# Optimization experiments

Hardware: AMD Instinct MI355X
Metric: run time of the kernel (lower is better)

The kernel has to match this reference:

```python
import jax, jax.numpy as jnp
import numpy as np

N, F = 8000, 256
NEG_SLOPE = 0.2


def setup_inputs() -> dict:
    key = jax.random.key(0)
    k1, k2, k3, k4, k5, k6, k7 = jax.random.split(key, 7)
    node_embeddings = jax.random.normal(k1, (N, F), dtype=jnp.float32)
    adj_matrix = jax.random.randint(k2, (N, N), 0, 2, dtype=jnp.int32)
    # Learned params: W (Linear F->F with bias), a (Linear 2F->1 with bias).
    # a's weight [1, 2F] is split into a_src (first F, applied to H_i) and
    # a_dst (last F, applied to H_j) -- mathematically identical to the
    # concat-then-linear formulation, without the N*N*2F intermediate.
    s = 1.0 / np.sqrt(F)
    W_w = jax.random.uniform(k3, (F, F), dtype=jnp.float32, minval=-s, maxval=s)
    W_b = jax.random.uniform(k4, (F,), dtype=jnp.float32, minval=-s, maxval=s)
    s2 = 1.0 / np.sqrt(2 * F)
    a_src = jax.random.uniform(k5, (F,), dtype=jnp.float32, minval=-s2, maxval=s2)
    a_dst = jax.random.uniform(k6, (F,), dtype=jnp.float32, minval=-s2, maxval=s2)
    a_b = jax.random.uniform(k7, (), dtype=jnp.float32, minval=-s2, maxval=s2)
    return {
        "node_embeddings": node_embeddings,
        "adj_matrix": adj_matrix,
        "W_w": W_w,
        "W_b": W_b,
        "a_src": a_src,
        "a_dst": a_dst,
        "a_b": a_b,
    }


def reference(node_embeddings, adj_matrix, W_w, W_b, a_src, a_dst, a_b):
    # H = W(x)
    H = node_embeddings @ W_w.T + W_b                      # [N, F]
    # e_ij = a([H_i ; H_j]) = H_i . a_src + H_j . a_dst + b
    e = (H @ a_src)[:, None] + (H @ a_dst)[None, :] + a_b  # [N, N]
    # mask BEFORE leakyrelu (as in the original), then leakyrelu, then softmax
    e = jnp.where(adj_matrix == 0, -jnp.inf, e)
    e = jnp.where(e >= 0, e, NEG_SLOPE * e)                # leakyrelu(-inf) = -inf
    attn = jax.nn.softmax(e, axis=1)                       # [N, N]
    return attn @ H                                        # [N, F]
```

## Files before the change

kernel.cpp:

```cpp
#include <hip/hip_runtime.h>

#define NN 8000
#define FD 256
#define NEG_SLOPE 0.2f
#define BM 64
#define KT 32
#define JCH 2048

typedef __bf16 bf16;
typedef __bf16 bf16x8 __attribute__((ext_vector_type(8)));
typedef __bf16 bf16x4 __attribute__((ext_vector_type(4)));
typedef float f32x4 __attribute__((ext_vector_type(4)));

__global__ __launch_bounds__(256) void k_linear(const float* __restrict__ X,
                                                const float* __restrict__ W,
                                                const float* __restrict__ b,
                                                bf16* __restrict__ Ht,
                                                float* __restrict__ out,
                                                float* __restrict__ lg) {
    __shared__ float Xs[16][260];
    const int t = threadIdx.x;
    const int i0 = blockIdx.x * 16;
    {
        const int gt = blockIdx.x * 256 + t;
        const float4 z4 = {0.f, 0.f, 0.f, 0.f};
        float4* o4 = (float4*)out;
        #pragma unroll
        for (int k = 0; k < 4; ++k) o4[gt + k * 128000] = z4;
        if (gt < NN) lg[gt] = 0.f;
    }
    #pragma unroll
    for (int r = 0; r < 16; ++r)
        Xs[r][t] = X[(size_t)(i0 + r) * FD + t];
    __syncthreads();
    const int f = t;
    float acc[16];
    const float bf_ = b[f];
    #pragma unroll
    for (int ii = 0; ii < 16; ++ii) acc[ii] = bf_;
    for (int k4 = 0; k4 < FD / 4; ++k4) {
        const float4 w4 = *(const float4*)&W[(size_t)f * FD + k4 * 4];
        #pragma unroll
        for (int ii = 0; ii < 16; ++ii) {
            const float4 x4 = *(const float4*)&Xs[ii][k4 * 4];
            acc[ii] += x4.x * w4.x + x4.y * w4.y + x4.z * w4.z + x4.w * w4.w;
        }
    }
    bf16x8 v0, v1;
    #pragma unroll
    for (int ii = 0; ii < 8; ++ii) { v0[ii] = (bf16)acc[ii]; v1[ii] = (bf16)acc[ii + 8]; }
    *(bf16x8*)&Ht[(size_t)f * NN + i0]     = v0;
    *(bf16x8*)&Ht[(size_t)f * NN + i0 + 8] = v1;
}

__global__ __launch_bounds__(256) void k_attn_vec(const bf16* __restrict__ Ht,
                                                  const float* __restrict__ a_src,
                                                  const float* __restrict__ a_dst,
                                                  const float* __restrict__ a_b,
                                                  float* __restrict__ hs,
                                                  float* __restrict__ hd) {
    __shared__ float psh[4][64], pdh[4][64];
    const int t = threadIdx.x;
    const int li = t & 63;
    const int q = t >> 6;
    const int i = blockIdx.x * 64 + li;
    float ps = 0.f, pd = 0.f;
    #pragma unroll 8
    for (int fi = 0; fi < 64; ++fi) {
        const int f = q * 64 + fi;
        const float h = (float)Ht[(size_t)f * NN + i];
        ps += h * a_src[f];
        pd += h * a_dst[f];
    }
    psh[q][li] = ps; pdh[q][li] = pd;
    __syncthreads();
    if (q == 0) {
        ps = psh[0][li] + psh[1][li] + psh[2][li] + psh[3][li];
        pd = pdh[0][li] + pdh[1][li] + pdh[2][li] + pdh[3][li];
        hs[i] = ps + a_b[0];
        hd[i] = pd;
    }
}

__global__ __launch_bounds__(512, 2) void k_gat(const bf16* __restrict__ Ht,
                                                const int* __restrict__ adj,
                                                const float* __restrict__ hs,
                                                const float* __restrict__ hd,
                                                float* __restrict__ out,
                                                float* __restrict__ lg) {
    __shared__ __attribute__((aligned(16))) bf16 Bt[2][FD * KT];
    __shared__ __attribute__((aligned(16))) int  Adt[3][BM * KT];
    __shared__ __attribute__((aligned(16))) bf16 Wt[2][BM * 40];
    __shared__ float hd_s[JCH];

    const int t  = threadIdx.x;
    const int l  = t & 63;
    const int wv = t >> 6;
    const int jb = blockIdx.x & 3;
    const int ib = blockIdx.x >> 2;
    const int i0 = ib * BM;
    const int j0 = jb * JCH;
    const int NS = (jb < 3) ? 64 : 58;

    const int r  = t >> 3;
    const int js = t & 7;
    const float hsv = hs[i0 + r];

    const int is = wv >> 2, fg = wv & 3;
    const int al = l & 15, asl = l >> 4;
    const int bswz = (asl ^ ((al >> 2) & 3)) << 4;

    auto stage_bt = [&](int s_, int buf) {
        #pragma unroll
        for (int q = 0; q < 2; ++q) {
            const int idx = q * 512 + t;
            const int col = idx >> 2, ks = idx & 3;
            const bf16* src = Ht + (size_t)col * NN + j0 + s_ * KT
                              + ((ks ^ ((col >> 2) & 3)) * 8);
            bf16* dst = &Bt[buf][idx * 8];
            __builtin_amdgcn_global_load_lds(
                (const __attribute__((address_space(1))) void*)src,
                (__attribute__((address_space(3))) void*)dst, 16, 0, 0);
        }
    };
    auto stage_ad = [&](int s_, int buf) {
        const int* src = adj + (size_t)(i0 + r) * NN + j0 + s_ * KT + js * 4;
        int* dst = &Adt[buf][t * 4];
        __builtin_amdgcn_global_load_lds(
            (const __attribute__((address_space(1))) void*)src,
            (__attribute__((address_space(3))) void*)dst, 16, 0, 0);
    };

    {
        const int jg = j0 + t * 4;
        float4 h4 = {0.f, 0.f, 0.f, 0.f};
        if (jg + 3 < NN) h4 = *(const float4*)(hd + jg);
        *(float4*)&hd_s[t * 4] = h4;
    }
    asm volatile("s_waitcnt vmcnt(0) lgkmcnt(0)" ::: "memory");
    stage_ad(0, 0);
    stage_bt(0, 0);
    stage_ad(1, 1);
    __builtin_amdgcn_s_barrier();

    f32x4 acc[2][4];
    #pragma unroll
    for (int rb = 0; rb < 2; ++rb)
        #pragma unroll
        for (int cf = 0; cf < 4; ++cf) acc[rb][cf] = (f32x4){0.f, 0.f, 0.f, 0.f};
    float lsum = 0.f;

    #pragma unroll 1
    for (int s = 0; s < NS; ++s) {
        const int bt = s & 1;
        if (s + 1 < NS) stage_bt(s + 1, (s + 1) & 1);
        if (s + 2 < NS) stage_ad(s + 2, (s + 2) % 3);
        if (s + 2 < NS)      asm volatile("s_waitcnt vmcnt(4)" ::: "memory");
        else if (s + 1 < NS) asm volatile("s_waitcnt vmcnt(3)" ::: "memory");
        else                 asm volatile("s_waitcnt vmcnt(0)" ::: "memory");

        {
            const int4 a4 = *(const int4*)&Adt[s % 3][t * 4];
            const float4 h4 = *(const float4*)&hd_s[s * KT + js * 4];
            float e, w0, w1, w2, w3;
            e = hsv + h4.x; e = fmaxf(e, NEG_SLOPE * e); w0 = a4.x ? __expf(e) : 0.f;
            e = hsv + h4.y; e = fmaxf(e, NEG_SLOPE * e); w1 = a4.y ? __expf(e) : 0.f;
            e = hsv + h4.z; e = fmaxf(e, NEG_SLOPE * e); w2 = a4.z ? __expf(e) : 0.f;
            e = hsv + h4.w; e = fmaxf(e, NEG_SLOPE * e); w3 = a4.w ? __expf(e) : 0.f;
            lsum += (w0 + w1) + (w2 + w3);
            bf16x4 w4v;
            w4v[0] = (bf16)w0; w4v[1] = (bf16)w1; w4v[2] = (bf16)w2; w4v[3] = (bf16)w3;
            *(bf16x4*)((char*)&Wt[bt][0] + r * 80 + js * 8) = w4v;
        }
        asm volatile("s_waitcnt lgkmcnt(0)" ::: "memory");
        __builtin_amdgcn_s_barrier();

        {
            const char* Ab = (const char*)&Wt[bt][0];
            const char* Bb = (const char*)&Bt[bt][0];
            bf16x8 a[2], b[4];
            #pragma unroll
            for (int rb = 0; rb < 2; ++rb)
                a[rb] = *(const bf16x8*)(Ab + (is * 32 + rb * 16 + al) * 80 + asl * 16);
            #pragma unroll
            for (int cf = 0; cf < 4; ++cf)
                b[cf] = *(const bf16x8*)(Bb + (fg * 64 + cf * 16 + al) * 64 + bswz);
            #pragma unroll
            for (int rb = 0; rb < 2; ++rb)
                #pragma unroll
                for (int cf = 0; cf < 4; ++cf)
                    acc[rb][cf] = __builtin_amdgcn_mfma_f32_16x16x32_bf16(
                        a[rb], b[cf], acc[rb][cf], 0, 0, 0);
        }
        asm volatile("s_waitcnt lgkmcnt(0)" ::: "memory");
        __builtin_amdgcn_s_barrier();
    }

    lsum += __shfl_xor(lsum, 1);
    lsum += __shfl_xor(lsum, 2);
    lsum += __shfl_xor(lsum, 4);
    if ((t & 7) == 0) atomicAdd(&lg[i0 + r], lsum);

    #pragma unroll
    for (int rb = 0; rb < 2; ++rb)
        #pragma unroll
        for (int cf = 0; cf < 4; ++cf)
            #pragma unroll
            for (int g = 0; g < 4; ++g)
                atomicAdd(&out[(size_t)(i0 + is * 32 + rb * 16 + asl * 4 + g) * FD
                               + fg * 64 + cf * 16 + al], acc[rb][cf][g]);
}

__global__ __launch_bounds__(256) void k_norm(float* __restrict__ out,
                                              const float* __restrict__ lg) {
    const int i = blockIdx.x;
    const float rinv = 1.0f / lg[i];
    out[(size_t)i * FD + threadIdx.x] *= rinv;
}

extern "C" void kernel_launch(void* const* d_in, const int* in_sizes, int n_in,
                              void* d_out, int out_size, void* d_ws, size_t ws_size,
                              hipStream_t stream) {
    const float* X     = (const float*)d_in[0];
    const int*   adj   = (const int*)d_in[1];
    const float* Ww    = (const float*)d_in[2];
    const float* Wb    = (const float*)d_in[3];
    const float* a_src = (const float*)d_in[4];
    const float* a_dst = (const float*)d_in[5];
    const float* a_b   = (const float*)d_in[6];
    float* out = (float*)d_out;

    bf16*  Ht = (bf16*)d_ws;
    float* hs = (float*)((char*)d_ws + (size_t)FD * NN * sizeof(bf16));
    float* hd = hs + NN;
    float* lg = hd + NN;

    k_linear<<<NN / 16, 256, 0, stream>>>(X, Ww, Wb, Ht, out, lg);
    k_attn_vec<<<NN / 64, 256, 0, stream>>>(Ht, a_src, a_dst, a_b, hs, hd);
    k_gat<<<125 * 4, 512, 0, stream>>>(Ht, adj, hs, hd, out, lg);
    k_norm<<<NN, 256, 0, stream>>>(out, lg);
}
```

Measured before the change: 151.8 us.

## Load Ht operands directly from global into registers instead of staging through LDS

```diff
diff --git a/kernel.cpp b/kernel.cpp
--- a/kernel.cpp
+++ b/kernel.cpp
@@ -88,7 +88,6 @@
                                                 const float* __restrict__ hd,
                                                 float* __restrict__ out,
                                                 float* __restrict__ lg) {
-    __shared__ __attribute__((aligned(16))) bf16 Bt[2][FD * KT];
     __shared__ __attribute__((aligned(16))) int  Adt[3][BM * KT];
     __shared__ __attribute__((aligned(16))) bf16 Wt[2][BM * 40];
     __shared__ float hd_s[JCH];
@@ -108,21 +107,12 @@
 
     const int is = wv >> 2, fg = wv & 3;
     const int al = l & 15, asl = l >> 4;
-    const int bswz = (asl ^ ((al >> 2) & 3)) << 4;
-
-    auto stage_bt = [&](int s_, int buf) {
-        #pragma unroll
-        for (int q = 0; q < 2; ++q) {
-            const int idx = q * 512 + t;
-            const int col = idx >> 2, ks = idx & 3;
-            const bf16* src = Ht + (size_t)col * NN + j0 + s_ * KT
-                              + ((ks ^ ((col >> 2) & 3)) * 8);
-            bf16* dst = &Bt[buf][idx * 8];
-            __builtin_amdgcn_global_load_lds(
-                (const __attribute__((address_space(1))) void*)src,
-                (__attribute__((address_space(3))) void*)dst, 16, 0, 0);
-        }
-    };
+
+    const bf16* bp0 = Ht + (size_t)(fg * 64 +  0 + al) * NN + j0 + asl * 8;
+    const bf16* bp1 = bp0 + (size_t)16 * NN;
+    const bf16* bp2 = bp0 + (size_t)32 * NN;
+    const bf16* bp3 = bp0 + (size_t)48 * NN;
+
     auto stage_ad = [&](int s_, int buf) {
         const int* src = adj + (size_t)(i0 + r) * NN + j0 + s_ * KT + js * 4;
         int* dst = &Adt[buf][t * 4];
@@ -139,7 +129,6 @@
     }
     asm volatile("s_waitcnt vmcnt(0) lgkmcnt(0)" ::: "memory");
     stage_ad(0, 0);
-    stage_bt(0, 0);
     stage_ad(1, 1);
     __builtin_amdgcn_s_barrier();
 
@@ -153,11 +142,15 @@
     #pragma unroll 1
     for (int s = 0; s < NS; ++s) {
         const int bt = s & 1;
-        if (s + 1 < NS) stage_bt(s + 1, (s + 1) & 1);
-        if (s + 2 < NS) stage_ad(s + 2, (s + 2) % 3);
-        if (s + 2 < NS)      asm volatile("s_waitcnt vmcnt(4)" ::: "memory");
-        else if (s + 1 < NS) asm volatile("s_waitcnt vmcnt(3)" ::: "memory");
-        else                 asm volatile("s_waitcnt vmcnt(0)" ::: "memory");
+
+        const size_t bo = (size_t)s * KT;
+        const bf16x8 b0 = *(const bf16x8*)(bp0 + bo);
+        const bf16x8 b1 = *(const bf16x8*)(bp1 + bo);
+        const bf16x8 b2 = *(const bf16x8*)(bp2 + bo);
+        const bf16x8 b3 = *(const bf16x8*)(bp3 + bo);
+        __builtin_amdgcn_sched_barrier(0);
+
+        asm volatile("s_waitcnt vmcnt(5)" ::: "memory");
 
         {
             const int4 a4 = *(const int4*)&Adt[s % 3][t * 4];
@@ -172,25 +165,26 @@
             w4v[0] = (bf16)w0; w4v[1] = (bf16)w1; w4v[2] = (bf16)w2; w4v[3] = (bf16)w3;
             *(bf16x4*)((char*)&Wt[bt][0] + r * 80 + js * 8) = w4v;
         }
+
+        if (s + 2 < NS) stage_ad(s + 2, (s + 2) % 3);
+
         asm volatile("s_waitcnt lgkmcnt(0)" ::: "memory");
         __builtin_amdgcn_s_barrier();
 
         {
             const char* Ab = (const char*)&Wt[bt][0];
-            const char* Bb = (const char*)&Bt[bt][0];
-            bf16x8 a[2], b[4];
+            bf16x8 a[2];
             #pragma unroll
             for (int rb = 0; rb < 2; ++rb)
                 a[rb] = *(const bf16x8*)(Ab + (is * 32 + rb * 16 + al) * 80 + asl * 16);
-            #pragma unroll
-            for (int cf = 0; cf < 4; ++cf)
-                b[cf] = *(const bf16x8*)(Bb + (fg * 64 + cf * 16 + al) * 64 + bswz);
-            #pragma unroll
-            for (int rb = 0; rb < 2; ++rb)
-                #pragma unroll
-                for (int cf = 0; cf < 4; ++cf)
-                    acc[rb][cf] = __builtin_amdgcn_mfma_f32_16x16x32_bf16(
-                        a[rb], b[cf], acc[rb][cf], 0, 0, 0);
+            acc[0][0] = __builtin_amdgcn_mfma_f32_16x16x32_bf16(a[0], b0, acc[0][0], 0, 0, 0);
+            acc[0][1] = __builtin_amdgcn_mfma_f32_16x16x32_bf16(a[0], b1, acc[0][1], 0, 0, 0);
+            acc[0][2] = __builtin_amdgcn_mfma_f32_16x16x32_bf16(a[0], b2, acc[0][2], 0, 0, 0);
+            acc[0][3] = __builtin_amdgcn_mfma_f32_16x16x32_bf16(a[0], b3, acc[0][3], 0, 0, 0);
+            acc[1][0] = __builtin_amdgcn_mfma_f32_16x16x32_bf16(a[1], b0, acc[1][0], 0, 0, 0);
+            acc[1][1] = __builtin_amdgcn_mfma_f32_16x16x32_bf16(a[1], b1, acc[1][1], 0, 0, 0);
+            acc[1][2] = __builtin_amdgcn_mfma_f32_16x16x32_bf16(a[1], b2, acc[1][2], 0, 0, 0);
+            acc[1][3] = __builtin_amdgcn_mfma_f32_16x16x32_bf16(a[1], b3, acc[1][3], 0, 0, 0);
         }
         asm volatile("s_waitcnt lgkmcnt(0)" ::: "memory");
         __builtin_amdgcn_s_barrier();
```

New measurement: 210.9 us. 1.39x slower.
